# Kernel tuning notes

Hardware: AMD Instinct MI355X
Metric: run time of the kernel (lower is better)

## Reference

```python
import jax, jax.numpy as jnp
import numpy as np

DT = 1.0
SEQ, BATCH, HID = 2048, 512, 256

def setup_inputs() -> dict:
    key = jax.random.key(0)
    ks = jax.random.split(key, 4)
    x = jax.random.normal(ks[0], (SEQ, BATCH, 1), dtype=jnp.float32)
    # small init scale keeps tanh unsaturated and the Euler recurrence stable
    W1 = 0.3 * jax.random.normal(ks[1], (2, HID), dtype=jnp.float32)
    b1 = jnp.zeros((HID,), jnp.float32)
    W2 = (0.3 / np.sqrt(HID)) * jax.random.normal(ks[2], (HID, HID), dtype=jnp.float32)
    b2 = jnp.zeros((HID,), jnp.float32)
    W3 = (0.1 / np.sqrt(HID)) * jax.random.normal(ks[3], (HID, 1), dtype=jnp.float32)
    b3 = jnp.zeros((1,), jnp.float32)
    state0 = jnp.zeros((BATCH,), jnp.float32)
    return {"x": x, "W1": W1, "b1": b1, "W2": W2, "b2": b2, "W3": W3, "b3": b3, "state0": state0}

def reference(x, W1, b1, W2, b2, W3, b3, state0):
    # Forward-Euler ODE integration: y[n+1] = y[n] + dt * f(x[n], y[n]).
    # Torch code returns odeint_output[:-1, :, None], i.e. the state at each
    # step BEFORE the update, with shape identical to x.
    xs = x[:, :, 0]  # (seq, batch) -- derivative_network.input = x.squeeze(2)

    def f(x_t, y):
        u = jnp.stack([x_t, y], axis=-1)          # (B, 2)
        h = jnp.tanh(u @ W1 + b1)                 # (B, H)
        h = jnp.tanh(h @ W2 + b2)                 # (B, H)
        return (h @ W3 + b3)[:, 0]                # (B,)

    def step(state, x_t):
        new_state = state + DT * f(x_t, state)
        return new_state, state                   # emit pre-update state

    _, ys = jax.lax.scan(step, state0, xs)        # ys: (seq, batch)
    return ys[:, :, None]                         # (seq, batch, 1), same shape as x
```

## Files before the change

### kernel.cpp

```cpp
#include <hip/hip_runtime.h>


#define SEQ 2048
#define BATCH 512
#define HID 256
#define LDA 288

typedef __bf16 bf16x8 __attribute__((ext_vector_type(8)));
typedef short short8 __attribute__((ext_vector_type(8)));
typedef float f32x4 __attribute__((ext_vector_type(4)));

__device__ __forceinline__ unsigned short f2bf_rne(float f) {
  unsigned u = __builtin_bit_cast(unsigned, f);
  u += 0x7fffu + ((u >> 16) & 1u);
  return (unsigned short)(u >> 16);
}

__device__ __forceinline__ float tanh_pade(float x) {
  float cx = __builtin_amdgcn_fmed3f(x, -4.5f, 4.5f);
  float u = cx * cx;
  float num = cx * (10395.f + u * (1260.f + 21.f * u));
  float den = 10395.f + u * (4725.f + u * (210.f + u));
  return num * __builtin_amdgcn_rcpf(den);
}

__device__ __forceinline__ float row16_sum_to_lane15(float v) {
  int s;
  s = __builtin_amdgcn_update_dpp(0, __builtin_bit_cast(int, v), 0x111, 0xf, 0xf, true);
  v += __builtin_bit_cast(float, s);
  s = __builtin_amdgcn_update_dpp(0, __builtin_bit_cast(int, v), 0x112, 0xf, 0xf, true);
  v += __builtin_bit_cast(float, s);
  s = __builtin_amdgcn_update_dpp(0, __builtin_bit_cast(int, v), 0x114, 0xf, 0xf, true);
  v += __builtin_bit_cast(float, s);
  s = __builtin_amdgcn_update_dpp(0, __builtin_bit_cast(int, v), 0x118, 0xf, 0xf, true);
  v += __builtin_bit_cast(float, s);
  return v;
}

__global__ void pack_w2_kernel(const float* __restrict__ W2,
                               unsigned short* __restrict__ ws) {
  int idx = blockIdx.x * 256 + threadIdx.x;
  int e    = idx & 7;
  int l    = (idx >> 3) & 63;
  int kc   = (idx >> 9) & 7;
  int tile = idx >> 12;
  int k = kc * 32 + (l >> 4) * 8 + e;
  int c = tile * 16 + (l & 15);
  ws[idx] = f2bf_rne(W2[k * HID + c]);
}

__global__ __launch_bounds__(256, 1) void odenet_kernel(
    const float* __restrict__ x, const float* __restrict__ W1,
    const float* __restrict__ b1, const unsigned short* __restrict__ wsW2,
    const float* __restrict__ b2, const float* __restrict__ W3,
    const float* __restrict__ b3, const float* __restrict__ state0,
    float* __restrict__ out) {
  __shared__ __align__(16) unsigned short A_lds[2 * LDA];
  __shared__ __align__(16) float partial[2][4];

  const int tid  = threadIdx.x;
  const int lane = tid & 63;
  const int wave = tid >> 6;
  const int j    = tid;
  const int b0   = blockIdx.x * 2;

  const float w10 = W1[j];
  const float w11 = W1[HID + j];
  const float b1j = b1[j];
  const float b3v = b3[0];
  float b2c[4], w3c[4];
#pragma unroll
  for (int t = 0; t < 4; ++t) {
    const int c = wave * 64 + t * 16 + (lane & 15);
    b2c[t] = b2[c];
    w3c[t] = W3[c];
  }

  short8 bf[4][8];
  {
    const short8* wp = (const short8*)wsW2;
#pragma unroll
    for (int t = 0; t < 4; ++t)
#pragma unroll
      for (int kc = 0; kc < 8; ++kc)
        bf[t][kc] = wp[((wave * 4 + t) * 8 + kc) * 64 + lane];
  }

  const int aoff = ((lane >> 2) & 1) * LDA + (lane >> 4) * 8;

  const f32x4 kZero = {0.f, 0.f, 0.f, 0.f};

  float y0 = state0[b0];
  float y1 = state0[b0 + 1];

  const float* xp = x + b0;
  float* yo = out + b0;

  float2 xb[8], xn[8];
  float xa0[8], xa1[8];
#pragma unroll
  for (int i = 0; i < 8; ++i) xb[i] = *(const float2*)&xp[i * BATCH];
#pragma unroll
  for (int i = 0; i < 8; ++i) {
    xa0[i] = xb[i].x * w10 + b1j;
    xa1[i] = xb[i].y * w10 + b1j;
  }

  if (tid < 8) ((float*)partial)[tid] = -0.25f * b3v;
  float base0 = __builtin_fmaf(y0, w11, xa0[0]);
  float base1 = __builtin_fmaf(y1, w11, xa1[0]);
  __syncthreads();

  for (int tb = 0; tb < SEQ; tb += 8) {
    if (tb + 8 < SEQ) {
      const float* xq = xp + (tb + 8) * BATCH;
#pragma unroll
      for (int i = 0; i < 8; ++i) xn[i] = *(const float2*)&xq[i * BATCH];
    }

#pragma unroll
    for (int i = 0; i < 8; ++i) {
      const int t = tb + i;

      const f32x4 q0 = *(const f32x4*)&partial[0][0];
      const f32x4 q1 = *(const f32x4*)&partial[1][0];
      const float f0 = ((q0[0] + q0[1]) + (q0[2] + q0[3])) + b3v;
      const float f1 = ((q1[0] + q1[1]) + (q1[2] + q1[3])) + b3v;

      const float pre0 = __builtin_fmaf(f0, w11, base0);
      const float pre1 = __builtin_fmaf(f1, w11, base1);
      A_lds[j]       = f2bf_rne(tanh_pade(pre0));
      A_lds[LDA + j] = f2bf_rne(tanh_pade(pre1));

      y0 += f0;
      y1 += f1;
      if (tid == 0) {
        float2 o{y0, y1};
        *(float2*)&yo[t * BATCH] = o;
      }
      {
        const float xaN0 = (i < 7) ? xa0[i + 1] : xn[0].x * w10 + b1j;
        const float xaN1 = (i < 7) ? xa1[i + 1] : xn[0].y * w10 + b1j;
        base0 = __builtin_fmaf(y0, w11, xaN0);
        base1 = __builtin_fmaf(y1, w11, xaN1);
      }
      __syncthreads();

      short8 areg[8];
#pragma unroll
      for (int kc = 0; kc < 8; ++kc)
        areg[kc] = *(const short8*)&A_lds[aoff + kc * 32];

      f32x4 acc0, acc1, acc2, acc3;
      {
        const bf16x8 a = __builtin_bit_cast(bf16x8, areg[0]);
        acc0 = __builtin_amdgcn_mfma_f32_16x16x32_bf16(a, __builtin_bit_cast(bf16x8, bf[0][0]), kZero, 0, 0, 0);
        acc1 = __builtin_amdgcn_mfma_f32_16x16x32_bf16(a, __builtin_bit_cast(bf16x8, bf[1][0]), kZero, 0, 0, 0);
      }
#pragma unroll
      for (int kc = 1; kc < 8; ++kc) {
        const bf16x8 a = __builtin_bit_cast(bf16x8, areg[kc]);
        acc0 = __builtin_amdgcn_mfma_f32_16x16x32_bf16(a, __builtin_bit_cast(bf16x8, bf[0][kc]), acc0, 0, 0, 0);
        acc1 = __builtin_amdgcn_mfma_f32_16x16x32_bf16(a, __builtin_bit_cast(bf16x8, bf[1][kc]), acc1, 0, 0, 0);
      }

      float s01 = tanh_pade(acc0[0] + b2c[0]) * w3c[0] +
                  tanh_pade(acc1[0] + b2c[1]) * w3c[1];

      {
        const bf16x8 a = __builtin_bit_cast(bf16x8, areg[0]);
        acc2 = __builtin_amdgcn_mfma_f32_16x16x32_bf16(a, __builtin_bit_cast(bf16x8, bf[2][0]), kZero, 0, 0, 0);
        acc3 = __builtin_amdgcn_mfma_f32_16x16x32_bf16(a, __builtin_bit_cast(bf16x8, bf[3][0]), kZero, 0, 0, 0);
      }
#pragma unroll
      for (int kc = 1; kc < 8; ++kc) {
        const bf16x8 a = __builtin_bit_cast(bf16x8, areg[kc]);
        acc2 = __builtin_amdgcn_mfma_f32_16x16x32_bf16(a, __builtin_bit_cast(bf16x8, bf[2][kc]), acc2, 0, 0, 0);
        acc3 = __builtin_amdgcn_mfma_f32_16x16x32_bf16(a, __builtin_bit_cast(bf16x8, bf[3][kc]), acc3, 0, 0, 0);
      }

      const float s23 = tanh_pade(acc2[0] + b2c[2]) * w3c[2] +
                        tanh_pade(acc3[0] + b2c[3]) * w3c[3];

      const float r = row16_sum_to_lane15(s01 + s23);
      if ((lane & 15) == 15 && lane < 32)
        partial[lane >> 4][wave] = r;
      __syncthreads();
    }

    if (tb + 8 < SEQ) {
#pragma unroll
      for (int i = 0; i < 8; ++i) xb[i] = xn[i];
#pragma unroll
      for (int i = 0; i < 8; ++i) {
        xa0[i] = xb[i].x * w10 + b1j;
        xa1[i] = xb[i].y * w10 + b1j;
      }
    }
  }
}

extern "C" void kernel_launch(void* const* d_in, const int* in_sizes, int n_in,
                              void* d_out, int out_size, void* d_ws, size_t ws_size,
                              hipStream_t stream) {
  const float* x  = (const float*)d_in[0];
  const float* W1 = (const float*)d_in[1];
  const float* b1 = (const float*)d_in[2];
  const float* W2 = (const float*)d_in[3];
  const float* b2 = (const float*)d_in[4];
  const float* W3 = (const float*)d_in[5];
  const float* b3 = (const float*)d_in[6];
  const float* s0 = (const float*)d_in[7];
  unsigned short* ws = (unsigned short*)d_ws;
  float* out = (float*)d_out;

  pack_w2_kernel<<<256, 256, 0, stream>>>(W2, ws);
  odenet_kernel<<<256, 256, 0, stream>>>(x, W1, b1, ws, b2, W3, b3, s0, out);
}
```

Before: 1.300 ms.

## Shorten serial step critical path and move state update off it

```diff
diff --git a/kernel.cpp b/kernel.cpp
--- a/kernel.cpp
+++ b/kernel.cpp
@@ -16,12 +16,9 @@
   return (unsigned short)(u >> 16);
 }
 
-__device__ __forceinline__ float tanh_pade(float x) {
-  float cx = __builtin_amdgcn_fmed3f(x, -4.5f, 4.5f);
-  float u = cx * cx;
-  float num = cx * (10395.f + u * (1260.f + 21.f * u));
-  float den = 10395.f + u * (4725.f + u * (210.f + u));
-  return num * __builtin_amdgcn_rcpf(den);
+__device__ __forceinline__ float tanh_e(float x) {
+  float t = __builtin_amdgcn_exp2f(x * 2.8853900817779268f);
+  return __builtin_fmaf(-2.f, __builtin_amdgcn_rcpf(t + 1.f), 1.f);
 }
 
 __device__ __forceinline__ float row16_sum_to_lane15(float v) {
@@ -107,8 +104,8 @@
   }
 
   if (tid < 8) ((float*)partial)[tid] = -0.25f * b3v;
-  float base0 = __builtin_fmaf(y0, w11, xa0[0]);
-  float base1 = __builtin_fmaf(y1, w11, xa1[0]);
+  float base0 = __builtin_fmaf(b3v, w11, __builtin_fmaf(y0, w11, xa0[0]));
+  float base1 = __builtin_fmaf(b3v, w11, __builtin_fmaf(y1, w11, xa1[0]));
   __syncthreads();
 
   for (int tb = 0; tb < SEQ; tb += 8) {
@@ -118,32 +115,18 @@
       for (int i = 0; i < 8; ++i) xn[i] = *(const float2*)&xq[i * BATCH];
     }
 
+    float2 yh[8];
+
 #pragma unroll
     for (int i = 0; i < 8; ++i) {
-      const int t = tb + i;
-
       const f32x4 q0 = *(const f32x4*)&partial[0][0];
       const f32x4 q1 = *(const f32x4*)&partial[1][0];
-      const float f0 = ((q0[0] + q0[1]) + (q0[2] + q0[3])) + b3v;
-      const float f1 = ((q1[0] + q1[1]) + (q1[2] + q1[3])) + b3v;
-
-      const float pre0 = __builtin_fmaf(f0, w11, base0);
-      const float pre1 = __builtin_fmaf(f1, w11, base1);
-      A_lds[j]       = f2bf_rne(tanh_pade(pre0));
-      A_lds[LDA + j] = f2bf_rne(tanh_pade(pre1));
-
-      y0 += f0;
-      y1 += f1;
-      if (tid == 0) {
-        float2 o{y0, y1};
-        *(float2*)&yo[t * BATCH] = o;
-      }
-      {
-        const float xaN0 = (i < 7) ? xa0[i + 1] : xn[0].x * w10 + b1j;
-        const float xaN1 = (i < 7) ? xa1[i + 1] : xn[0].y * w10 + b1j;
-        base0 = __builtin_fmaf(y0, w11, xaN0);
-        base1 = __builtin_fmaf(y1, w11, xaN1);
-      }
+      const float s0sum = (q0[0] + q0[1]) + (q0[2] + q0[3]);
+      const float s1sum = (q1[0] + q1[1]) + (q1[2] + q1[3]);
+      const float pre0 = __builtin_fmaf(s0sum, w11, base0);
+      const float pre1 = __builtin_fmaf(s1sum, w11, base1);
+      A_lds[j]       = f2bf_rne(tanh_e(pre0));
+      A_lds[LDA + j] = f2bf_rne(tanh_e(pre1));
       __syncthreads();
 
       short8 areg[8];
@@ -164,8 +147,19 @@
         acc1 = __builtin_amdgcn_mfma_f32_16x16x32_bf16(a, __builtin_bit_cast(bf16x8, bf[1][kc]), acc1, 0, 0, 0);
       }
 
-      float s01 = tanh_pade(acc0[0] + b2c[0]) * w3c[0] +
-                  tanh_pade(acc1[0] + b2c[1]) * w3c[1];
+      y0 += s0sum + b3v;
+      y1 += s1sum + b3v;
+      yh[i] = float2{y0, y1};
+      {
+        const float xaN0 = (i < 7) ? xa0[i + 1] : xn[0].x * w10 + b1j;
+        const float xaN1 = (i < 7) ? xa1[i + 1] : xn[0].y * w10 + b1j;
+        base0 = __builtin_fmaf(b3v, w11, __builtin_fmaf(y0, w11, xaN0));
+        base1 = __builtin_fmaf(b3v, w11, __builtin_fmaf(y1, w11, xaN1));
+      }
+
+      const float s01 = tanh_e(acc0[0] + b2c[0]) * w3c[0] +
+                        tanh_e(acc1[0] + b2c[1]) * w3c[1];
+      const float r01 = row16_sum_to_lane15(s01);
 
       {
         const bf16x8 a = __builtin_bit_cast(bf16x8, areg[0]);
@@ -179,13 +173,19 @@
         acc3 = __builtin_amdgcn_mfma_f32_16x16x32_bf16(a, __builtin_bit_cast(bf16x8, bf[3][kc]), acc3, 0, 0, 0);
       }
 
-      const float s23 = tanh_pade(acc2[0] + b2c[2]) * w3c[2] +
-                        tanh_pade(acc3[0] + b2c[3]) * w3c[3];
-
-      const float r = row16_sum_to_lane15(s01 + s23);
+      const float s23 = tanh_e(acc2[0] + b2c[2]) * w3c[2] +
+                        tanh_e(acc3[0] + b2c[3]) * w3c[3];
+      const float r = row16_sum_to_lane15(s23) + r01;
+
       if ((lane & 15) == 15 && lane < 32)
         partial[lane >> 4][wave] = r;
       __syncthreads();
+    }
+
+    if (tid == 0) {
+#pragma unroll
+      for (int i = 0; i < 8; ++i)
+        *(float2*)&yo[(tb + i) * BATCH] = yh[i];
     }
 
     if (tb + 8 < SEQ) {
```

New measurement: 1.306 ms. No clear change (+0.4%).
